# Optimization experiments

Hardware: AMD Instinct MI355X
Metric: run time of the kernel (lower is better)

## Reference

```python
import jax, jax.numpy as jnp
import numpy as np

B, CI, CO, A = 2048, 32, 32, 16   # batch, caps_in, caps_out, atom
ITER_NUM = 5


def setup_inputs() -> dict:
    key = jax.random.key(0)
    k1, = jax.random.split(key, 1)
    x = jax.random.normal(k1, (B, CI, CO, A), dtype=jnp.float32)
    gamma = jnp.ones((1, CI, 1, A), dtype=jnp.float32)
    beta = jnp.zeros((1, CI, 1, A), dtype=jnp.float32)
    return {"x": x, "gamma": gamma, "beta": beta}


def _iter_norm_inv_sqrt(sigma, iter_num):
    # sigma: [CI, A, A] batched covariance; Newton-Schulz inverse square root.
    a = sigma.shape[-1]
    trace = jnp.trace(sigma, axis1=-2, axis2=-1)[:, None, None]  # [CI,1,1]
    sigma_n = sigma / trace                                      # trace-normalize
    p = jnp.broadcast_to(jnp.eye(a, dtype=sigma.dtype), sigma.shape)
    for _ in range(iter_num):
        p = 0.5 * (3.0 * p - p @ p @ p @ sigma_n)
    return p / jnp.sqrt(trace)


def reference(x, gamma, beta):
    b, ci, co, a = x.shape
    # center over batch and caps_out axes (axes [0, 2])
    mean = jnp.mean(x, axis=(0, 2), keepdims=True)                # [1,CI,1,A]
    centered = x - mean
    # [CI, B*CO, A]
    c = jnp.transpose(centered, (1, 0, 2, 3)).reshape(ci, b * co, a)
    # per-capsule covariance, normalized by (batch*caps_out - 1)
    sigma = jnp.einsum('cna,cnb->cab', c, c) / (jnp.float32(b * co) - 1.0)
    w = _iter_norm_inv_sqrt(sigma, ITER_NUM)                       # [CI,A,A]
    dec = jnp.einsum('cna,cab->cnb', c, w)                         # whiten
    dec = jnp.transpose(dec.reshape(ci, b, co, a), (1, 0, 2, 3))   # [B,CI,CO,A]
    return dec * gamma + beta
```

## Files before the change

### kernel.cpp

```cpp
#include <hip/hip_runtime.h>
#include <math.h>

constexpr int CI = 32;
constexpr int CO = 32;
constexpr int A  = 16;
constexpr float INV_N   = 1.0f / 65536.0f;
constexpr float INV_NM1 = 1.0f / 65535.0f;

constexpr int NCHUNK = 32;
constexpr int PART_STRIDE = 272;

constexpr int WS_PART = 0;
constexpr int WS_W    = CI * NCHUNK * PART_STRIDE;

__global__ __launch_bounds__(256) void k_stats(const float* __restrict__ x,
                                               float* __restrict__ ws) {
    const int ci    = blockIdx.x & 31;
    const int chunk = blockIdx.x >> 5;
    const int tid   = threadIdx.x;
    const int sub   = tid & 3;
    const int quad  = tid >> 2;

    float acc[4][16];
    float sacc[4];
#pragma unroll
    for (int i = 0; i < 4; ++i) {
        sacc[i] = 0.0f;
#pragma unroll
        for (int b2 = 0; b2 < 16; ++b2) acc[i][b2] = 0.0f;
    }

    const int n_base = chunk * 2048;
    for (int it = 0; it < 32; ++it) {
        const int n  = n_base + it * 64 + quad;
        const int b  = n >> 5;
        const int co = n & 31;
        const float* vptr = x + ((size_t)(b * CI + ci) * CO + co) * A;

        float v[16];
#pragma unroll
        for (int j = 0; j < 4; ++j) {
            const float4 f = *reinterpret_cast<const float4*>(vptr + j * 4);
            v[4 * j + 0] = f.x; v[4 * j + 1] = f.y;
            v[4 * j + 2] = f.z; v[4 * j + 3] = f.w;
        }
        const float4 fa = *reinterpret_cast<const float4*>(vptr + sub * 4);
        const float va[4] = {fa.x, fa.y, fa.z, fa.w};

#pragma unroll
        for (int i = 0; i < 4; ++i) {
            sacc[i] += va[i];
#pragma unroll
            for (int b2 = 0; b2 < 16; ++b2) acc[i][b2] += va[i] * v[b2];
        }
    }

#pragma unroll
    for (int m = 4; m < 64; m <<= 1) {
#pragma unroll
        for (int i = 0; i < 4; ++i) {
            sacc[i] += __shfl_xor(sacc[i], m, 64);
#pragma unroll
            for (int b2 = 0; b2 < 16; ++b2)
                acc[i][b2] += __shfl_xor(acc[i][b2], m, 64);
        }
    }

    __shared__ float red[4][272];
    const int wv = tid >> 6;
    if ((tid & 63) < 4) {
#pragma unroll
        for (int i = 0; i < 4; ++i) {
#pragma unroll
            for (int b2 = 0; b2 < 16; ++b2)
                red[wv][sub * 68 + i * 16 + b2] = acc[i][b2];
            red[wv][sub * 68 + 64 + i] = sacc[i];
        }
    }
    __syncthreads();
    float* slot = ws + WS_PART + (ci * NCHUNK + chunk) * PART_STRIDE;
    for (int e = tid; e < 272; e += 256) {
        slot[e] = red[0][e] + red[1][e] + red[2][e] + red[3][e];
    }
}

__global__ __launch_bounds__(256) void k_ns(float* __restrict__ ws) {
    const int ci  = blockIdx.x;
    const int tid = threadIdx.x;
    const int r = tid >> 4, c = tid & 15;

    __shared__ float red2[272];
    __shared__ float sig[16][17];
    __shared__ float p[16][17];
    __shared__ float t1[16][17];
    __shared__ float t2[16][17];
    __shared__ float trace_s;

    const float* base = ws + WS_PART + (size_t)ci * NCHUNK * PART_STRIDE;
    for (int e = tid; e < 272; e += 256) {
        float s = 0.0f;
#pragma unroll
        for (int ch = 0; ch < NCHUNK; ++ch)
            s += base[ch * PART_STRIDE + e];
        red2[e] = s;
    }
    __syncthreads();

    const float P_rc = red2[(r >> 2) * 68 + ((r & 3) << 4) + c];
    const float S_r  = red2[(r >> 2) * 68 + 64 + (r & 3)];
    const float S_c  = red2[(c >> 2) * 68 + 64 + (c & 3)];
    sig[r][c] = (P_rc - S_r * S_c * INV_N) * INV_NM1;
    __syncthreads();

    if (tid == 0) {
        float tr = 0.0f;
        for (int i = 0; i < 16; ++i) tr += sig[i][i];
        trace_s = tr;
    }
    __syncthreads();
    const float tr = trace_s;

    sig[r][c] = sig[r][c] / tr;
    p[r][c]   = (r == c) ? 1.0f : 0.0f;
    __syncthreads();

    for (int it = 0; it < 5; ++it) {
        float a = 0.0f;
        for (int k = 0; k < 16; ++k) a += p[r][k] * p[k][c];
        t1[r][c] = a;
        __syncthreads();
        float b2 = 0.0f;
        for (int k = 0; k < 16; ++k) b2 += t1[r][k] * p[k][c];
        t2[r][c] = b2;
        __syncthreads();
        float d = 0.0f;
        for (int k = 0; k < 16; ++k) d += t2[r][k] * sig[k][c];
        const float np = 0.5f * (3.0f * p[r][c] - d);
        __syncthreads();
        p[r][c] = np;
        __syncthreads();
    }

    ws[WS_W + ci * 256 + r * 16 + c] = p[r][c] / sqrtf(tr);
    if (tid < 16) {
        ws[WS_W + CI * 256 + ci * 16 + tid] =
            red2[(tid >> 2) * 68 + 64 + (tid & 3)];
    }
}

__global__ __launch_bounds__(256) void k_apply(const float* __restrict__ x,
                                               const float* __restrict__ gamma,
                                               const float* __restrict__ beta,
                                               const float* __restrict__ ws,
                                               float* __restrict__ out) {
    const int ci    = blockIdx.x & 31;
    const int chunk = blockIdx.x >> 5;
    const int tid   = threadIdx.x;
    const int sub   = tid & 3;
    const int quad  = tid >> 2;
    const int b0    = sub * 4;

    const float* W = ws + WS_W + ci * 256;
    const float* S = ws + WS_W + CI * 256 + ci * 16;

    float g[4], c0[4];
#pragma unroll
    for (int i = 0; i < 4; ++i) g[i] = gamma[ci * 16 + b0 + i];

    float wg[16][4];
    float bias[4] = {0.0f, 0.0f, 0.0f, 0.0f};
#pragma unroll
    for (int a = 0; a < 16; ++a) {
        const float4 wr = *reinterpret_cast<const float4*>(W + a * 16 + b0);
        const float m = S[a] * INV_N;
        wg[a][0] = wr.x * g[0]; wg[a][1] = wr.y * g[1];
        wg[a][2] = wr.z * g[2]; wg[a][3] = wr.w * g[3];
        bias[0] += m * wr.x; bias[1] += m * wr.y;
        bias[2] += m * wr.z; bias[3] += m * wr.w;
    }
#pragma unroll
    for (int i = 0; i < 4; ++i)
        c0[i] = beta[ci * 16 + b0 + i] - bias[i] * g[i];

    const int n_base = chunk * 1024;
    for (int it = 0; it < 16; ++it) {
        const int n  = n_base + it * 64 + quad;
        const int b  = n >> 5;
        const int co = n & 31;
        const size_t voff = ((size_t)(b * CI + ci) * CO + co) * A;
        const float* vptr = x + voff;

        float v[16];
#pragma unroll
        for (int j = 0; j < 4; ++j) {
            const float4 f = *reinterpret_cast<const float4*>(vptr + j * 4);
            v[4 * j + 0] = f.x; v[4 * j + 1] = f.y;
            v[4 * j + 2] = f.z; v[4 * j + 3] = f.w;
        }

        float acc[4] = {c0[0], c0[1], c0[2], c0[3]};
#pragma unroll
        for (int a = 0; a < 16; ++a) {
#pragma unroll
            for (int i = 0; i < 4; ++i) acc[i] += v[a] * wg[a][i];
        }

        float4 o;
        o.x = acc[0]; o.y = acc[1]; o.z = acc[2]; o.w = acc[3];
        *reinterpret_cast<float4*>(out + voff + b0) = o;
    }
}

extern "C" void kernel_launch(void* const* d_in, const int* in_sizes, int n_in,
                              void* d_out, int out_size, void* d_ws, size_t ws_size,
                              hipStream_t stream) {
    const float* x     = (const float*)d_in[0];
    const float* gamma = (const float*)d_in[1];
    const float* beta  = (const float*)d_in[2];
    float* out = (float*)d_out;
    float* ws  = (float*)d_ws;

    k_stats<<<dim3(1024), dim3(256), 0, stream>>>(x, ws);
    k_ns<<<dim3(32), dim3(256), 0, stream>>>(ws);
    k_apply<<<dim3(2048), dim3(256), 0, stream>>>(x, gamma, beta, ws, out);
}
```

Before: 90.69 us.

## Fold Newton-Schulz solve into apply kernel and use nontemporal output stores

Removes the separate single-wave k_ns launch. Every apply block now reduces the 32 partial statistics itself and runs the 5-iteration Newton-Schulz inverse square root in shared memory, then uses the resulting matrix directly. The apply grid is halved to 1024 blocks, each covering twice as many rows, which amortises the redundant solve. Output is written with nontemporal stores to reduce cache pollution. In exchange, each block repeats a small serial, sync-heavy matrix computation before streaming, which delays the start of the memory traffic.

```diff
diff --git a/kernel.cpp b/kernel.cpp
--- a/kernel.cpp
+++ b/kernel.cpp
@@ -3,7 +3,6 @@
 
 constexpr int CI = 32;
 constexpr int CO = 32;
-constexpr int A  = 16;
 constexpr float INV_N   = 1.0f / 65536.0f;
 constexpr float INV_NM1 = 1.0f / 65535.0f;
 
@@ -11,7 +10,8 @@
 constexpr int PART_STRIDE = 272;
 
 constexpr int WS_PART = 0;
-constexpr int WS_W    = CI * NCHUNK * PART_STRIDE;
+
+using f32x4 = __attribute__((ext_vector_type(4))) float;
 
 __global__ __launch_bounds__(256) void k_stats(const float* __restrict__ x,
                                                float* __restrict__ ws) {
@@ -35,7 +35,7 @@
         const int n  = n_base + it * 64 + quad;
         const int b  = n >> 5;
         const int co = n & 31;
-        const float* vptr = x + ((size_t)(b * CI + ci) * CO + co) * A;
+        const float* vptr = x + ((size_t)(b * CI + ci) * CO + co) * 16;
 
         float v[16];
 #pragma unroll
@@ -81,70 +81,6 @@
     float* slot = ws + WS_PART + (ci * NCHUNK + chunk) * PART_STRIDE;
     for (int e = tid; e < 272; e += 256) {
         slot[e] = red[0][e] + red[1][e] + red[2][e] + red[3][e];
-    }
-}
-
-__global__ __launch_bounds__(256) void k_ns(float* __restrict__ ws) {
-    const int ci  = blockIdx.x;
-    const int tid = threadIdx.x;
-    const int r = tid >> 4, c = tid & 15;
-
-    __shared__ float red2[272];
-    __shared__ float sig[16][17];
-    __shared__ float p[16][17];
-    __shared__ float t1[16][17];
-    __shared__ float t2[16][17];
-    __shared__ float trace_s;
-
-    const float* base = ws + WS_PART + (size_t)ci * NCHUNK * PART_STRIDE;
-    for (int e = tid; e < 272; e += 256) {
-        float s = 0.0f;
-#pragma unroll
-        for (int ch = 0; ch < NCHUNK; ++ch)
-            s += base[ch * PART_STRIDE + e];
-        red2[e] = s;
-    }
-    __syncthreads();
-
-    const float P_rc = red2[(r >> 2) * 68 + ((r & 3) << 4) + c];
-    const float S_r  = red2[(r >> 2) * 68 + 64 + (r & 3)];
-    const float S_c  = red2[(c >> 2) * 68 + 64 + (c & 3)];
-    sig[r][c] = (P_rc - S_r * S_c * INV_N) * INV_NM1;
-    __syncthreads();
-
-    if (tid == 0) {
-        float tr = 0.0f;
-        for (int i = 0; i < 16; ++i) tr += sig[i][i];
-        trace_s = tr;
-    }
-    __syncthreads();
-    const float tr = trace_s;
-
-    sig[r][c] = sig[r][c] / tr;
-    p[r][c]   = (r == c) ? 1.0f : 0.0f;
-    __syncthreads();
-
-    for (int it = 0; it < 5; ++it) {
-        float a = 0.0f;
-        for (int k = 0; k < 16; ++k) a += p[r][k] * p[k][c];
-        t1[r][c] = a;
-        __syncthreads();
-        float b2 = 0.0f;
-        for (int k = 0; k < 16; ++k) b2 += t1[r][k] * p[k][c];
-        t2[r][c] = b2;
-        __syncthreads();
-        float d = 0.0f;
-        for (int k = 0; k < 16; ++k) d += t2[r][k] * sig[k][c];
-        const float np = 0.5f * (3.0f * p[r][c] - d);
-        __syncthreads();
-        p[r][c] = np;
-        __syncthreads();
-    }
-
-    ws[WS_W + ci * 256 + r * 16 + c] = p[r][c] / sqrtf(tr);
-    if (tid < 16) {
-        ws[WS_W + CI * 256 + ci * 16 + tid] =
-            red2[(tid >> 2) * 68 + 64 + (tid & 3)];
     }
 }
 
@@ -158,10 +94,62 @@
     const int tid   = threadIdx.x;
     const int sub   = tid & 3;
     const int quad  = tid >> 2;
-    const int b0    = sub * 4;
-
-    const float* W = ws + WS_W + ci * 256;
-    const float* S = ws + WS_W + CI * 256 + ci * 16;
+    const int r = tid >> 4, c = tid & 15;
+
+    __shared__ float red2[272];
+    __shared__ float sig[16][17];
+    __shared__ float pm[16][17];
+    __shared__ float t1[16][17];
+    __shared__ float t2[16][17];
+    __shared__ float trace_s;
+
+    const float* base = ws + WS_PART + (size_t)ci * NCHUNK * PART_STRIDE;
+    for (int e = tid; e < 272; e += 256) {
+        float s = 0.0f;
+#pragma unroll
+        for (int ch = 0; ch < NCHUNK; ++ch)
+            s += base[ch * PART_STRIDE + e];
+        red2[e] = s;
+    }
+    __syncthreads();
+
+    const float P_rc = red2[(r >> 2) * 68 + ((r & 3) << 4) + c];
+    const float S_r  = red2[(r >> 2) * 68 + 64 + (r & 3)];
+    const float S_c  = red2[(c >> 2) * 68 + 64 + (c & 3)];
+    sig[r][c] = (P_rc - S_r * S_c * INV_N) * INV_NM1;
+    __syncthreads();
+
+    if (tid == 0) {
+        float tr = 0.0f;
+        for (int i = 0; i < 16; ++i) tr += sig[i][i];
+        trace_s = tr;
+    }
+    __syncthreads();
+    const float tr = trace_s;
+
+    sig[r][c] = sig[r][c] / tr;
+    pm[r][c]  = (r == c) ? 1.0f : 0.0f;
+    __syncthreads();
+
+    for (int it = 0; it < 5; ++it) {
+        float a = 0.0f;
+        for (int k = 0; k < 16; ++k) a += pm[r][k] * pm[k][c];
+        t1[r][c] = a;
+        __syncthreads();
+        float b2 = 0.0f;
+        for (int k = 0; k < 16; ++k) b2 += t1[r][k] * pm[k][c];
+        t2[r][c] = b2;
+        __syncthreads();
+        float d = 0.0f;
+        for (int k = 0; k < 16; ++k) d += t2[r][k] * sig[k][c];
+        const float np = 0.5f * (3.0f * pm[r][c] - d);
+        __syncthreads();
+        pm[r][c] = np;
+        __syncthreads();
+    }
+    const float inv_sqrt_tr = 1.0f / sqrtf(tr);
+
+    const int b0 = sub * 4;
 
     float g[4], c0[4];
 #pragma unroll
@@ -171,23 +159,24 @@
     float bias[4] = {0.0f, 0.0f, 0.0f, 0.0f};
 #pragma unroll
     for (int a = 0; a < 16; ++a) {
-        const float4 wr = *reinterpret_cast<const float4*>(W + a * 16 + b0);
-        const float m = S[a] * INV_N;
-        wg[a][0] = wr.x * g[0]; wg[a][1] = wr.y * g[1];
-        wg[a][2] = wr.z * g[2]; wg[a][3] = wr.w * g[3];
-        bias[0] += m * wr.x; bias[1] += m * wr.y;
-        bias[2] += m * wr.z; bias[3] += m * wr.w;
+        const float m = red2[(a >> 2) * 68 + 64 + (a & 3)] * INV_N;
+#pragma unroll
+        for (int i = 0; i < 4; ++i) {
+            const float w = pm[a][b0 + i] * inv_sqrt_tr;
+            wg[a][i] = w * g[i];
+            bias[i] += m * w;
+        }
     }
 #pragma unroll
     for (int i = 0; i < 4; ++i)
         c0[i] = beta[ci * 16 + b0 + i] - bias[i] * g[i];
 
-    const int n_base = chunk * 1024;
-    for (int it = 0; it < 16; ++it) {
+    const int n_base = chunk * 2048;
+    for (int it = 0; it < 32; ++it) {
         const int n  = n_base + it * 64 + quad;
         const int b  = n >> 5;
         const int co = n & 31;
-        const size_t voff = ((size_t)(b * CI + ci) * CO + co) * A;
+        const size_t voff = ((size_t)(b * CI + ci) * CO + co) * 16;
         const float* vptr = x + voff;
 
         float v[16];
@@ -198,16 +187,16 @@
             v[4 * j + 2] = f.z; v[4 * j + 3] = f.w;
         }
 
-        float acc[4] = {c0[0], c0[1], c0[2], c0[3]};
+        float oacc[4] = {c0[0], c0[1], c0[2], c0[3]};
 #pragma unroll
         for (int a = 0; a < 16; ++a) {
 #pragma unroll
-            for (int i = 0; i < 4; ++i) acc[i] += v[a] * wg[a][i];
-        }
-
-        float4 o;
-        o.x = acc[0]; o.y = acc[1]; o.z = acc[2]; o.w = acc[3];
-        *reinterpret_cast<float4*>(out + voff + b0) = o;
+            for (int i = 0; i < 4; ++i) oacc[i] += v[a] * wg[a][i];
+        }
+
+        f32x4 o;
+        o.x = oacc[0]; o.y = oacc[1]; o.z = oacc[2]; o.w = oacc[3];
+        __builtin_nontemporal_store(o, reinterpret_cast<f32x4*>(out + voff + b0));
     }
 }
 
@@ -221,6 +210,5 @@
     float* ws  = (float*)d_ws;
 
     k_stats<<<dim3(1024), dim3(256), 0, stream>>>(x, ws);
-    k_ns<<<dim3(32), dim3(256), 0, stream>>>(ws);
-    k_apply<<<dim3(2048), dim3(256), 0, stream>>>(x, gamma, beta, ws, out);
+    k_apply<<<dim3(1024), dim3(256), 0, stream>>>(x, gamma, beta, ws, out);
 }
```

After: 92.61 us. +2.1%, slower.
